# Kernel optimization log

Measured on AMD Instinct MI355X. Metric: run time of the kernel, lower is better.

## Reference

```python
import jax, jax.numpy as jnp
import numpy as np

STATE_DIM = 256
ACTION_DIM = 2
HIDDEN = 512
N_HEADS = 5          # per ensemble; 2*N_HEADS stacked critics total
CEM_POP = 4096
CEM_ITERS = 4
ELITE_N = max(1, int(round(CEM_POP * 0.2)))  # 819
ACTION_LOW, ACTION_HIGH = -1.0, 1.0
INIT_STD, MIN_STD = 0.4, 0.1


def setup_inputs() -> dict:
    key = jax.random.key(0)
    ks = jax.random.split(key, 6)
    in_dim = STATE_DIM + ACTION_DIM
    state = jax.random.normal(ks[0], (1, STATE_DIM), dtype=jnp.float32)
    noise = jax.random.normal(ks[1], (CEM_ITERS, CEM_POP, ACTION_DIM), dtype=jnp.float32)
    W1 = jax.random.normal(ks[2], (2 * N_HEADS, in_dim, HIDDEN), dtype=jnp.float32) / np.sqrt(in_dim).astype(np.float32)
    b1 = jnp.zeros((2 * N_HEADS, HIDDEN), dtype=jnp.float32)
    W2 = jax.random.normal(ks[3], (2 * N_HEADS, HIDDEN, HIDDEN), dtype=jnp.float32) / np.sqrt(HIDDEN).astype(np.float32)
    b2 = jnp.zeros((2 * N_HEADS, HIDDEN), dtype=jnp.float32)
    W3 = jax.random.normal(ks[4], (2 * N_HEADS, HIDDEN, 1), dtype=jnp.float32) / np.sqrt(HIDDEN).astype(np.float32)
    b3 = jnp.zeros((2 * N_HEADS, 1), dtype=jnp.float32)
    return {"state": state, "noise": noise, "W1": W1, "b1": b1, "W2": W2, "b2": b2, "W3": W3, "b3": b3}


def _ensemble_scores(s_batch, a, W1, b1, W2, b2, W3, b3):
    # x: [P, state+action]; heads stacked on leading dim h = 2*N_HEADS
    x = jnp.concatenate([s_batch, a], axis=-1)
    h = jax.nn.relu(jnp.einsum('pi,hij->hpj', x, W1) + b1[:, None, :])
    h = jax.nn.relu(jnp.einsum('hpj,hjk->hpk', h, W2) + b2[:, None, :])
    q = (jnp.einsum('hpk,hko->hpo', h, W3) + b3[:, None, :])[..., 0]  # [2H, P]
    q1, q2 = q[:N_HEADS], q[N_HEADS:]
    return jnp.minimum(q1, q2).mean(axis=0)  # [P]


def reference(state, noise, W1, b1, W2, b2, W3, b3):
    s = state[0]  # squeeze(0)
    s_batch = jnp.broadcast_to(s, (CEM_POP, STATE_DIM))

    def step(carry, eps):
        mu, std, best_a, best_score = carry
        a = jnp.clip(mu + std * eps, ACTION_LOW, ACTION_HIGH)  # [P, A]
        scores = _ensemble_scores(s_batch, a, W1, b1, W2, b2, W3, b3)
        vals, idx = jax.lax.top_k(scores, ELITE_N)
        elite = a[idx]  # [ELITE_N, A]
        mu2 = elite.mean(axis=0)
        std2 = jnp.maximum(jnp.std(elite, axis=0, ddof=1), MIN_STD)  # torch unbiased std
        better = vals[0] > best_score
        best_a2 = jnp.where(better, elite[0], best_a)
        best_score2 = jnp.where(better, vals[0], best_score)
        return (mu2, std2, best_a2, best_score2), None

    carry0 = (jnp.zeros((ACTION_DIM,), jnp.float32),
              jnp.full((ACTION_DIM,), INIT_STD, jnp.float32),
              jnp.zeros((ACTION_DIM,), jnp.float32),
              jnp.float32(-jnp.inf))
    (mu, std, best_a, best_score), _ = jax.lax.scan(step, carry0, noise)
    return best_a[None, :]  # [1, ACTION_DIM]
```

## Files before the change

### kernel.cpp

```cpp
#include <hip/hip_runtime.h>
#include <math.h>

#define SDIM   256
#define HID    512
#define NH     5
#define HEADS  10
#define POP    4096
#define ITERS  4
#define ELITE  819
#define INIT_STDF 0.4f
#define MIN_STDF  0.1f

#define WS_BASE1 0
#define WS_Q     5120
#define WS_STATE 87040
#define WS_W2S_BYTE 348224
#define W2S_USHORTS (HEADS * 2 * 16 * 16384)
#define WS_NEED_BYTES (WS_W2S_BYTE + (size_t)W2S_USHORTS * 2)

typedef __attribute__((ext_vector_type(4))) float f32x4;
typedef __attribute__((ext_vector_type(8))) short bf16x8;

static __device__ __forceinline__ unsigned short bf16_rne(float x) {
    unsigned b = __float_as_uint(x);
    return (unsigned short)((b + 0x7FFFu + ((b >> 16) & 1u)) >> 16);
}

static __device__ __forceinline__ unsigned pack2(float x, float y) {
    unsigned r;
    asm("v_cvt_pk_bf16_f32 %0, %1, %2" : "=v"(r) : "v"(x), "v"(y));
    return r;
}

static __device__ __forceinline__ float clip1(float x) {
    return fminf(fmaxf(x, -1.f), 1.f);
}

__global__ __launch_bounds__(256) void k_base(const float* __restrict__ state,
                                              const float* __restrict__ W1,
                                              const float* __restrict__ b1,
                                              float* __restrict__ ws)
{
    const int h = blockIdx.y;
    const int j = blockIdx.x * 256 + threadIdx.x;
    const float* w1h = W1 + (size_t)h * 258 * HID;
    float acc = b1[h * HID + j];
    for (int i = 0; i < SDIM; ++i)
        acc += state[i] * w1h[(size_t)i * HID + j];
    ws[WS_BASE1 + h * HID + j] = acc;

    if (h == 0 && blockIdx.x == 0 && threadIdx.x == 0) {
        float* st = ws + WS_STATE;
        st[0] = 0.f; st[1] = 0.f;
        st[2] = INIT_STDF; st[3] = INIT_STDF;
        st[4] = 0.f; st[5] = 0.f;
        st[6] = -3.402823466e38f;
    }
}

__global__ __launch_bounds__(256) void k_split(const float* __restrict__ W2,
                                               unsigned short* __restrict__ W2S)
{
    const int h = blockIdx.z, cb = blockIdx.y, jc = blockIdx.x;
    const int c = threadIdx.x;
    unsigned short* slab = W2S + (size_t)((h * 2 + cb) * 16 + jc) * 16384;
    #pragma unroll
    for (int jg = 0; jg < 4; ++jg) {
        unsigned hp[4], lp[4];
        #pragma unroll
        for (int i = 0; i < 4; ++i) {
            const int j = jc * 32 + jg * 8 + 2 * i;
            float v0 = W2[(size_t)(h * HID + j) * HID + cb * 256 + c];
            float v1 = W2[(size_t)(h * HID + j + 1) * HID + cb * 256 + c];
            unsigned short h0 = bf16_rne(v0), h1 = bf16_rne(v1);
            float f0 = __uint_as_float((unsigned)h0 << 16);
            float f1 = __uint_as_float((unsigned)h1 << 16);
            unsigned short l0 = bf16_rne(v0 - f0), l1 = bf16_rne(v1 - f1);
            hp[i] = (unsigned)h0 | ((unsigned)h1 << 16);
            lp[i] = (unsigned)l0 | ((unsigned)l1 << 16);
        }
        uint4 HV, LV;
        HV.x = hp[0]; HV.y = hp[1]; HV.z = hp[2]; HV.w = hp[3];
        LV.x = lp[0]; LV.y = lp[1]; LV.z = lp[2]; LV.w = lp[3];
        *(uint4*)&slab[jg * 2048 + c * 8] = HV;
        *(uint4*)&slab[8192 + jg * 2048 + c * 8] = LV;
    }
}

__global__ __launch_bounds__(512, 4) void k_score_mfma7(
    const float* __restrict__ noise, const float* __restrict__ W1,
    const unsigned short* __restrict__ W2S,
    const float* __restrict__ b2, const float* __restrict__ W3,
    float* __restrict__ ws, int t)
{
    __shared__ unsigned short As[2][4096];
    __shared__ float red[8][64];

    const int tid = threadIdx.x;
    const int bid = blockIdx.x;
    const int w = (bid & 7) * 160 + (bid >> 3);
    const int h = w >> 7;
    const int rem = w & 127;
    const int cb = rem >> 6;
    const int rs = rem & 63;

    const int lane = tid & 63;
    const int wv = tid >> 6;
    const int l15 = lane & 15, lk = lane >> 4;

    const int arow = tid & 63;
    const int akg = (tid >> 6) & 3;

    const float* st = ws + WS_STATE;
    const float mu0 = st[0], mu1 = st[1], sd0 = st[2], sd1 = st[3];
    float2 e = *(const float2*)&noise[((size_t)t * POP + rs * 64 + arow) * 2];
    const float a0 = clip1(mu0 + sd0 * e.x);
    const float a1 = clip1(mu1 + sd1 * e.y);

    const float* base1 = ws + WS_BASE1 + h * HID;
    const float* w1u = W1 + ((size_t)h * 258 + 256) * HID;
    const float* w1v = W1 + ((size_t)h * 258 + 257) * HID;
    const unsigned short* bslab = W2S + (size_t)((h * 2 + cb) * 16) * 16384;
    const int bco = lk * 2048 + (wv * 32 + l15) * 8;

    auto computeA = [&](int jc, int buf) {
        if (tid < 256) {
            const int j = jc * 32 + akg * 8;
            f32x4 b0 = *(const f32x4*)&base1[j];
            f32x4 b1v = *(const f32x4*)&base1[j + 4];
            f32x4 u0 = *(const f32x4*)&w1u[j];
            f32x4 u1 = *(const f32x4*)&w1u[j + 4];
            f32x4 v0 = *(const f32x4*)&w1v[j];
            f32x4 v1 = *(const f32x4*)&w1v[j + 4];
            float hv[8];
            #pragma unroll
            for (int i = 0; i < 4; ++i) {
                hv[i]     = fmaxf(b0[i] + a0 * u0[i] + a1 * v0[i], 0.f);
                hv[4 + i] = fmaxf(b1v[i] + a0 * u1[i] + a1 * v1[i], 0.f);
            }
            unsigned ph[4], pl[4];
            #pragma unroll
            for (int i = 0; i < 4; ++i) {
                ph[i] = pack2(hv[2 * i], hv[2 * i + 1]);
                float fx = __uint_as_float(ph[i] << 16);
                float fy = __uint_as_float(ph[i] & 0xFFFF0000u);
                pl[i] = pack2(hv[2 * i] - fx, hv[2 * i + 1] - fy);
            }
            uint4 HV, LV;
            HV.x = ph[0]; HV.y = ph[1]; HV.z = ph[2]; HV.w = ph[3];
            LV.x = pl[0]; LV.y = pl[1]; LV.z = pl[2]; LV.w = pl[3];
            *(uint4*)&As[buf][akg * 512 + arow * 8] = HV;
            *(uint4*)&As[buf][2048 + akg * 512 + arow * 8] = LV;
        }
    };

    f32x4 acc[4][2];
    #pragma unroll
    for (int m = 0; m < 4; ++m)
        #pragma unroll
        for (int n = 0; n < 2; ++n)
            acc[m][n] = (f32x4){0.f, 0.f, 0.f, 0.f};

    computeA(0, 0);
    bf16x8 BH[2], BL[2];
    #pragma unroll
    for (int n = 0; n < 2; ++n) {
        BH[n] = *(const bf16x8*)(bslab + bco + n * 128);
        BL[n] = *(const bf16x8*)(bslab + 8192 + bco + n * 128);
    }
    __syncthreads();

    int cur = 0;
    #pragma unroll 1
    for (int kc = 0; kc < 16; ++kc) {
        bf16x8 AH[4], AL[4];
        #pragma unroll
        for (int m = 0; m < 4; ++m) {
            const int ad = lk * 512 + (m * 16 + l15) * 8;
            AH[m] = *(const bf16x8*)&As[cur][ad];
            AL[m] = *(const bf16x8*)&As[cur][2048 + ad];
        }
        const int nc = (kc < 15) ? kc + 1 : 15;
        const unsigned short* bnc = bslab + (size_t)nc * 16384;
        bf16x8 nBH[2], nBL[2];
        #pragma unroll
        for (int n = 0; n < 2; ++n) {
            nBH[n] = *(const bf16x8*)(bnc + bco + n * 128);
            nBL[n] = *(const bf16x8*)(bnc + 8192 + bco + n * 128);
        }
        __builtin_amdgcn_s_setprio(1);
        #pragma unroll
        for (int m = 0; m < 4; ++m)
            #pragma unroll
            for (int n = 0; n < 2; ++n)
                acc[m][n] = __builtin_amdgcn_mfma_f32_16x16x32_bf16(
                    AH[m], BH[n], acc[m][n], 0, 0, 0);
        #pragma unroll
        for (int m = 0; m < 4; ++m)
            #pragma unroll
            for (int n = 0; n < 2; ++n)
                acc[m][n] = __builtin_amdgcn_mfma_f32_16x16x32_bf16(
                    AL[m], BH[n], acc[m][n], 0, 0, 0);
        #pragma unroll
        for (int m = 0; m < 4; ++m)
            #pragma unroll
            for (int n = 0; n < 2; ++n)
                acc[m][n] = __builtin_amdgcn_mfma_f32_16x16x32_bf16(
                    AH[m], BL[n], acc[m][n], 0, 0, 0);
        __builtin_amdgcn_s_setprio(0);
        computeA(nc, cur ^ 1);
        __syncthreads();
        #pragma unroll
        for (int n = 0; n < 2; ++n) { BH[n] = nBH[n]; BL[n] = nBL[n]; }
        cur ^= 1;
    }

    float qp[4][4];
    #pragma unroll
    for (int m = 0; m < 4; ++m)
        #pragma unroll
        for (int r = 0; r < 4; ++r) qp[m][r] = 0.f;
    #pragma unroll
    for (int n = 0; n < 2; ++n) {
        int gcol = cb * 256 + wv * 32 + n * 16 + l15;
        float b2v = b2[h * HID + gcol];
        float w3v = W3[h * HID + gcol];
        #pragma unroll
        for (int m = 0; m < 4; ++m)
            #pragma unroll
            for (int r = 0; r < 4; ++r)
                qp[m][r] += fmaxf(acc[m][n][r] + b2v, 0.f) * w3v;
    }
    #pragma unroll
    for (int m = 0; m < 4; ++m)
        #pragma unroll
        for (int r = 0; r < 4; ++r) {
            float v = qp[m][r];
            v += __shfl_xor(v, 1);
            v += __shfl_xor(v, 2);
            v += __shfl_xor(v, 4);
            v += __shfl_xor(v, 8);
            if (l15 == 0) red[wv][m * 16 + lk * 4 + r] = v;
        }
    __syncthreads();
    if (tid < 64) {
        float q = 0.f;
        #pragma unroll
        for (int s = 0; s < 8; ++s) q += red[s][tid];
        ws[WS_Q + (size_t)(cb * HEADS + h) * POP + rs * 64 + tid] = q;
    }
}

__global__ __launch_bounds__(256) void k_score(const float* __restrict__ noise,
                                               const float* __restrict__ W1,
                                               const float* __restrict__ W2,
                                               const float* __restrict__ b2,
                                               const float* __restrict__ W3,
                                               float* __restrict__ ws, int t)
{
    __shared__ float h1[32][HID];
    __shared__ float a0s[32], a1s[32];
    __shared__ float red[2][16][2];

    const int tid = threadIdx.x;
    const int h   = blockIdx.y;
    const int p0  = blockIdx.x * 32;

    if (tid < 32) {
        const float* st = ws + WS_STATE;
        const int p = p0 + tid;
        float e0 = noise[((size_t)t * POP + p) * 2 + 0];
        float e1 = noise[((size_t)t * POP + p) * 2 + 1];
        a0s[tid] = fminf(fmaxf(st[0] + st[2] * e0, -1.f), 1.f);
        a1s[tid] = fminf(fmaxf(st[1] + st[3] * e1, -1.f), 1.f);
    }
    __syncthreads();

    const float* base1 = ws + WS_BASE1 + h * HID;
    const float* w1u = W1 + ((size_t)h * 258 + 256) * HID;
    const float* w1v = W1 + ((size_t)h * 258 + 257) * HID;
    #pragma unroll
    for (int jj = 0; jj < 2; ++jj) {
        int j = tid + jj * 256;
        float bb = base1[j], uu = w1u[j], vv = w1v[j];
        #pragma unroll
        for (int p = 0; p < 32; ++p)
            h1[p][j] = fmaxf(bb + a0s[p] * uu + a1s[p] * vv, 0.f);
    }
    __syncthreads();

    const int pg = tid >> 7;
    const int kl = tid & 127;
    const float* W2h = W2 + (size_t)h * HID * HID + kl;

    float acc[16][4];
    #pragma unroll
    for (int p = 0; p < 16; ++p)
        #pragma unroll
        for (int dk = 0; dk < 4; ++dk) acc[p][dk] = 0.f;

    for (int j0 = 0; j0 < HID; j0 += 4) {
        float w[4][4];
        #pragma unroll
        for (int dj = 0; dj < 4; ++dj)
            #pragma unroll
            for (int dk = 0; dk < 4; ++dk)
                w[dj][dk] = W2h[(size_t)(j0 + dj) * HID + dk * 128];
        #pragma unroll
        for (int p = 0; p < 16; ++p) {
            const float4 hv = *(const float4*)&h1[pg * 16 + p][j0];
            #pragma unroll
            for (int dk = 0; dk < 4; ++dk)
                acc[p][dk] += hv.x * w[0][dk] + hv.y * w[1][dk]
                            + hv.z * w[2][dk] + hv.w * w[3][dk];
        }
    }

    float b2v[4], w3v[4];
    #pragma unroll
    for (int dk = 0; dk < 4; ++dk) {
        b2v[dk] = b2[h * HID + kl + dk * 128];
        w3v[dk] = W3[h * HID + kl + dk * 128];
    }
    const int wid  = tid >> 6;
    const int lane = tid & 63;
    const int wig  = wid & 1;
    #pragma unroll
    for (int p = 0; p < 16; ++p) {
        float v = 0.f;
        #pragma unroll
        for (int dk = 0; dk < 4; ++dk)
            v += fmaxf(acc[p][dk] + b2v[dk], 0.f) * w3v[dk];
        #pragma unroll
        for (int off = 32; off; off >>= 1) v += __shfl_down(v, off);
        if (lane == 0) red[pg][p][wig] = v;
    }
    __syncthreads();
    if (tid < 32) {
        int pp = tid & 15, g = tid >> 4;
        ws[WS_Q + (size_t)h * POP + p0 + g * 16 + pp] =
            red[g][pp][0] + red[g][pp][1];
        ws[WS_Q + (size_t)(HEADS + h) * POP + p0 + g * 16 + pp] = 0.f;
    }
}

__global__ __launch_bounds__(256) void k_select(const float* __restrict__ noise,
                                                const float* __restrict__ b3,
                                                float* __restrict__ ws,
                                                float* __restrict__ out, int t)
{
    __shared__ float    sc[POP];
    __shared__ unsigned uk[POP];
    __shared__ unsigned hist[256];
    __shared__ int      scan[256];
    __shared__ float    rf[256];
    __shared__ int      ri_[256];
    __shared__ double   rd[256];
    __shared__ unsigned s_prefix;
    __shared__ int      s_r;

    const int tid = threadIdx.x;
    const float* q = ws + WS_Q;
    float* st = ws + WS_STATE;
    const float mu0 = st[0], mu1 = st[1], sd0 = st[2], sd1 = st[3];

    #pragma unroll
    for (int g = 0; g < 4; ++g) {
        const int p = g * 1024 + tid * 4;
        f32x4 s = (f32x4){0.f, 0.f, 0.f, 0.f};
        #pragma unroll
        for (int hh = 0; hh < NH; ++hh) {
            f32x4 qa0 = *(const f32x4*)&q[(size_t)hh * POP + p];
            f32x4 qa1 = *(const f32x4*)&q[(size_t)(HEADS + hh) * POP + p];
            f32x4 qb0 = *(const f32x4*)&q[(size_t)(NH + hh) * POP + p];
            f32x4 qb1 = *(const f32x4*)&q[(size_t)(HEADS + NH + hh) * POP + p];
            float ba = b3[hh], bb = b3[NH + hh];
            #pragma unroll
            for (int i = 0; i < 4; ++i)
                s[i] += fminf(qa0[i] + qa1[i] + ba, qb0[i] + qb1[i] + bb);
        }
        #pragma unroll
        for (int i = 0; i < 4; ++i) {
            float v = s[i] * 0.2f;
            sc[p + i] = v;
            unsigned b = __float_as_uint(v);
            uk[p + i] = (b & 0x80000000u) ? ~b : (b | 0x80000000u);
        }
    }
    __syncthreads();

    float mv = -3.402823466e38f; int mi = 0;
    for (int p = tid; p < POP; p += 256) {
        float v = sc[p];
        if (v > mv) { mv = v; mi = p; }
    }
    rf[tid] = mv; ri_[tid] = mi;
    __syncthreads();
    for (int off = 128; off; off >>= 1) {
        if (tid < off) {
            float ov = rf[tid + off]; int oi = ri_[tid + off];
            if (ov > rf[tid] || (ov == rf[tid] && oi < ri_[tid])) {
                rf[tid] = ov; ri_[tid] = oi;
            }
        }
        __syncthreads();
    }
    const float maxsc = rf[0];
    const int argmax = ri_[0];
    __syncthreads();

    unsigned prefix = 0; int r = ELITE;
    for (int shift = 24; shift >= 0; shift -= 8) {
        hist[tid] = 0;
        __syncthreads();
        const unsigned himask = (shift < 24) ? (0xFFFFFFFFu << (shift + 8)) : 0u;
        for (int p = tid; p < POP; p += 256) {
            unsigned key = uk[p];
            if ((key & himask) == prefix)
                atomicAdd(&hist[(key >> shift) & 255u], 1u);
        }
        __syncthreads();
        scan[tid] = (int)hist[tid];
        __syncthreads();
        for (int off = 1; off < 256; off <<= 1) {
            int v = (tid + off < 256) ? scan[tid + off] : 0;
            __syncthreads();
            scan[tid] += v;
            __syncthreads();
        }
        int above = (tid < 255) ? scan[tid + 1] : 0;
        if (scan[tid] >= r && above < r) {
            s_prefix = prefix | ((unsigned)tid << shift);
            s_r = r - above;
        }
        __syncthreads();
        prefix = s_prefix; r = s_r;
        __syncthreads();
    }
    const unsigned uT = prefix;
    const int take = r;

    int tieloc = 0;
    {
        const int base = tid * 16;
        #pragma unroll
        for (int k = 0; k < 16; ++k) if (uk[base + k] == uT) tieloc++;
    }
    scan[tid] = tieloc;
    __syncthreads();
    for (int off = 1; off < 256; off <<= 1) {
        int v = (tid >= off) ? scan[tid - off] : 0;
        __syncthreads();
        scan[tid] += v;
        __syncthreads();
    }
    const int tieExcl = scan[tid] - tieloc;

    double s0 = 0, s1 = 0, ss0 = 0, ss1 = 0;
    {
        const int base = tid * 16;
        int trank = tieExcl;
        for (int k = 0; k < 16; ++k) {
            const int p = base + k;
            const unsigned key = uk[p];
            bool inc = false;
            if (key > uT) inc = true;
            else if (key == uT) { if (trank < take) inc = true; trank++; }
            if (inc) {
                float e0 = noise[((size_t)t * POP + p) * 2 + 0];
                float e1 = noise[((size_t)t * POP + p) * 2 + 1];
                float a0 = fminf(fmaxf(mu0 + sd0 * e0, -1.f), 1.f);
                float a1 = fminf(fmaxf(mu1 + sd1 * e1, -1.f), 1.f);
                s0 += a0; s1 += a1;
                ss0 += (double)a0 * a0; ss1 += (double)a1 * a1;
            }
        }
    }
    double S0, S1, SS0, SS1;
    rd[tid] = s0;  __syncthreads();
    for (int off = 128; off; off >>= 1) { if (tid < off) rd[tid] += rd[tid + off]; __syncthreads(); }
    S0 = rd[0]; __syncthreads();
    rd[tid] = s1;  __syncthreads();
    for (int off = 128; off; off >>= 1) { if (tid < off) rd[tid] += rd[tid + off]; __syncthreads(); }
    S1 = rd[0]; __syncthreads();
    rd[tid] = ss0; __syncthreads();
    for (int off = 128; off; off >>= 1) { if (tid < off) rd[tid] += rd[tid + off]; __syncthreads(); }
    SS0 = rd[0]; __syncthreads();
    rd[tid] = ss1; __syncthreads();
    for (int off = 128; off; off >>= 1) { if (tid < off) rd[tid] += rd[tid + off]; __syncthreads(); }
    SS1 = rd[0]; __syncthreads();

    if (tid == 0) {
        const double n = (double)ELITE;
        double m0 = S0 / n, m1 = S1 / n;
        double v0 = (SS0 - S0 * S0 / n) / (n - 1.0);
        double v1 = (SS1 - S1 * S1 / n) / (n - 1.0);
        float nsd0 = fmaxf((float)sqrt(fmax(v0, 0.0)), MIN_STDF);
        float nsd1 = fmaxf((float)sqrt(fmax(v1, 0.0)), MIN_STDF);
        float e0 = noise[((size_t)t * POP + argmax) * 2 + 0];
        float e1 = noise[((size_t)t * POP + argmax) * 2 + 1];
        float a0 = fminf(fmaxf(mu0 + sd0 * e0, -1.f), 1.f);
        float a1 = fminf(fmaxf(mu1 + sd1 * e1, -1.f), 1.f);
        if (maxsc > st[6]) { st[4] = a0; st[5] = a1; st[6] = maxsc; }
        st[0] = (float)m0; st[1] = (float)m1; st[2] = nsd0; st[3] = nsd1;
        if (t == ITERS - 1) { out[0] = st[4]; out[1] = st[5]; }
    }
}

extern "C" void kernel_launch(void* const* d_in, const int* in_sizes, int n_in,
                              void* d_out, int out_size, void* d_ws, size_t ws_size,
                              hipStream_t stream)
{
    const float* state = (const float*)d_in[0];
    const float* noise = (const float*)d_in[1];
    const float* W1    = (const float*)d_in[2];
    const float* b1    = (const float*)d_in[3];
    const float* W2    = (const float*)d_in[4];
    const float* b2    = (const float*)d_in[5];
    const float* W3    = (const float*)d_in[6];
    const float* b3    = (const float*)d_in[7];
    float* out = (float*)d_out;
    float* ws  = (float*)d_ws;

    const bool fast = ws_size >= WS_NEED_BYTES;

    k_base<<<dim3(2, HEADS), 256, 0, stream>>>(state, W1, b1, ws);
    if (fast) {
        unsigned short* W2S = (unsigned short*)((char*)d_ws + WS_W2S_BYTE);
        k_split<<<dim3(16, 2, HEADS), 256, 0, stream>>>(W2, W2S);
        for (int t = 0; t < ITERS; ++t) {
            k_score_mfma7<<<dim3(1280), 512, 0, stream>>>(
                noise, W1, W2S, b2, W3, ws, t);
            k_select<<<1, 256, 0, stream>>>(noise, b3, ws, out, t);
        }
    } else {
        for (int t = 0; t < ITERS; ++t) {
            k_score<<<dim3(POP / 32, HEADS), 256, 0, stream>>>(noise, W1, W2, b2, W3, ws, t);
            k_select<<<1, 256, 0, stream>>>(noise, b3, ws, out, t);
        }
    }
}
```

Before: 344.3 us.

## Switch scoring GEMM to 32x32x16 MFMA and widen select kernel to 1024 threads

The scoring kernel's inner product moves from 16x16x32 bf16 MFMA tiles to 32x32x16 tiles. It uses 16-wide accumulators and new A/B fragment addressing, which cuts the number of MFMA issues and LDS fragment loads per K-chunk. The epilogue reduction adds one more shuffle stage and remaps rows to fit the 32x32 output layout. Separately, the single-block top-k/select kernel grows from 256 to 1024 threads so each thread does less serial work, at the cost of longer scans and reductions and heavier barriers.

```diff
diff --git a/kernel.cpp b/kernel.cpp
--- a/kernel.cpp
+++ b/kernel.cpp
@@ -19,6 +19,7 @@
 #define WS_NEED_BYTES (WS_W2S_BYTE + (size_t)W2S_USHORTS * 2)
 
 typedef __attribute__((ext_vector_type(4))) float f32x4;
+typedef __attribute__((ext_vector_type(16))) float f32x16;
 typedef __attribute__((ext_vector_type(8))) short bf16x8;
 
 static __device__ __forceinline__ unsigned short bf16_rne(float x) {
@@ -87,7 +88,7 @@
     }
 }
 
-__global__ __launch_bounds__(512, 4) void k_score_mfma7(
+__global__ __launch_bounds__(512, 4) void k_score_mfma8(
     const float* __restrict__ noise, const float* __restrict__ W1,
     const unsigned short* __restrict__ W2S,
     const float* __restrict__ b2, const float* __restrict__ W3,
@@ -106,7 +107,8 @@
 
     const int lane = tid & 63;
     const int wv = tid >> 6;
-    const int l15 = lane & 15, lk = lane >> 4;
+    const int l31 = lane & 31;
+    const int lg = lane >> 5;
 
     const int arow = tid & 63;
     const int akg = (tid >> 6) & 3;
@@ -121,7 +123,8 @@
     const float* w1u = W1 + ((size_t)h * 258 + 256) * HID;
     const float* w1v = W1 + ((size_t)h * 258 + 257) * HID;
     const unsigned short* bslab = W2S + (size_t)((h * 2 + cb) * 16) * 16384;
-    const int bco = lk * 2048 + (wv * 32 + l15) * 8;
+    const int bco = lg * 2048 + (wv * 32 + l31) * 8;
+    const int ar0 = lg * 512 + l31 * 8;
 
     auto computeA = [&](int jc, int buf) {
         if (tid < 256) {
@@ -154,93 +157,83 @@
         }
     };
 
-    f32x4 acc[4][2];
-    #pragma unroll
-    for (int m = 0; m < 4; ++m)
-        #pragma unroll
-        for (int n = 0; n < 2; ++n)
-            acc[m][n] = (f32x4){0.f, 0.f, 0.f, 0.f};
+    f32x16 acc[2];
+    #pragma unroll
+    for (int mi = 0; mi < 2; ++mi)
+        #pragma unroll
+        for (int i = 0; i < 16; ++i) acc[mi][i] = 0.f;
 
     computeA(0, 0);
     bf16x8 BH[2], BL[2];
     #pragma unroll
-    for (int n = 0; n < 2; ++n) {
-        BH[n] = *(const bf16x8*)(bslab + bco + n * 128);
-        BL[n] = *(const bf16x8*)(bslab + 8192 + bco + n * 128);
+    for (int ks = 0; ks < 2; ++ks) {
+        BH[ks] = *(const bf16x8*)(bslab + bco + ks * 4096);
+        BL[ks] = *(const bf16x8*)(bslab + 8192 + bco + ks * 4096);
     }
     __syncthreads();
 
     int cur = 0;
     #pragma unroll 1
     for (int kc = 0; kc < 16; ++kc) {
-        bf16x8 AH[4], AL[4];
-        #pragma unroll
-        for (int m = 0; m < 4; ++m) {
-            const int ad = lk * 512 + (m * 16 + l15) * 8;
-            AH[m] = *(const bf16x8*)&As[cur][ad];
-            AL[m] = *(const bf16x8*)&As[cur][2048 + ad];
-        }
+        bf16x8 AH[2][2], AL[2][2];
+        #pragma unroll
+        for (int ks = 0; ks < 2; ++ks)
+            #pragma unroll
+            for (int mi = 0; mi < 2; ++mi) {
+                const int ad = ar0 + ks * 1024 + mi * 256;
+                AH[ks][mi] = *(const bf16x8*)&As[cur][ad];
+                AL[ks][mi] = *(const bf16x8*)&As[cur][2048 + ad];
+            }
         const int nc = (kc < 15) ? kc + 1 : 15;
         const unsigned short* bnc = bslab + (size_t)nc * 16384;
         bf16x8 nBH[2], nBL[2];
         #pragma unroll
-        for (int n = 0; n < 2; ++n) {
-            nBH[n] = *(const bf16x8*)(bnc + bco + n * 128);
-            nBL[n] = *(const bf16x8*)(bnc + 8192 + bco + n * 128);
+        for (int ks = 0; ks < 2; ++ks) {
+            nBH[ks] = *(const bf16x8*)(bnc + bco + ks * 4096);
+            nBL[ks] = *(const bf16x8*)(bnc + 8192 + bco + ks * 4096);
         }
         __builtin_amdgcn_s_setprio(1);
         #pragma unroll
-        for (int m = 0; m < 4; ++m)
-            #pragma unroll
-            for (int n = 0; n < 2; ++n)
-                acc[m][n] = __builtin_amdgcn_mfma_f32_16x16x32_bf16(
-                    AH[m], BH[n], acc[m][n], 0, 0, 0);
-        #pragma unroll
-        for (int m = 0; m < 4; ++m)
-            #pragma unroll
-            for (int n = 0; n < 2; ++n)
-                acc[m][n] = __builtin_amdgcn_mfma_f32_16x16x32_bf16(
-                    AL[m], BH[n], acc[m][n], 0, 0, 0);
-        #pragma unroll
-        for (int m = 0; m < 4; ++m)
-            #pragma unroll
-            for (int n = 0; n < 2; ++n)
-                acc[m][n] = __builtin_amdgcn_mfma_f32_16x16x32_bf16(
-                    AH[m], BL[n], acc[m][n], 0, 0, 0);
+        for (int ks = 0; ks < 2; ++ks)
+            #pragma unroll
+            for (int mi = 0; mi < 2; ++mi)
+                acc[mi] = __builtin_amdgcn_mfma_f32_32x32x16_bf16(
+                    AH[ks][mi], BH[ks], acc[mi], 0, 0, 0);
+        #pragma unroll
+        for (int ks = 0; ks < 2; ++ks)
+            #pragma unroll
+            for (int mi = 0; mi < 2; ++mi)
+                acc[mi] = __builtin_amdgcn_mfma_f32_32x32x16_bf16(
+                    AL[ks][mi], BH[ks], acc[mi], 0, 0, 0);
+        #pragma unroll
+        for (int ks = 0; ks < 2; ++ks)
+            #pragma unroll
+            for (int mi = 0; mi < 2; ++mi)
+                acc[mi] = __builtin_amdgcn_mfma_f32_32x32x16_bf16(
+                    AH[ks][mi], BL[ks], acc[mi], 0, 0, 0);
         __builtin_amdgcn_s_setprio(0);
         computeA(nc, cur ^ 1);
         __syncthreads();
         #pragma unroll
-        for (int n = 0; n < 2; ++n) { BH[n] = nBH[n]; BL[n] = nBL[n]; }
+        for (int ks = 0; ks < 2; ++ks) { BH[ks] = nBH[ks]; BL[ks] = nBL[ks]; }
         cur ^= 1;
     }
 
-    float qp[4][4];
-    #pragma unroll
-    for (int m = 0; m < 4; ++m)
-        #pragma unroll
-        for (int r = 0; r < 4; ++r) qp[m][r] = 0.f;
-    #pragma unroll
-    for (int n = 0; n < 2; ++n) {
-        int gcol = cb * 256 + wv * 32 + n * 16 + l15;
-        float b2v = b2[h * HID + gcol];
-        float w3v = W3[h * HID + gcol];
-        #pragma unroll
-        for (int m = 0; m < 4; ++m)
-            #pragma unroll
-            for (int r = 0; r < 4; ++r)
-                qp[m][r] += fmaxf(acc[m][n][r] + b2v, 0.f) * w3v;
-    }
-    #pragma unroll
-    for (int m = 0; m < 4; ++m)
-        #pragma unroll
-        for (int r = 0; r < 4; ++r) {
-            float v = qp[m][r];
+    const int gcol = cb * 256 + wv * 32 + l31;
+    const float b2v = b2[h * HID + gcol];
+    const float w3v = W3[h * HID + gcol];
+    #pragma unroll
+    for (int mi = 0; mi < 2; ++mi)
+        #pragma unroll
+        for (int r = 0; r < 16; ++r) {
+            float v = fmaxf(acc[mi][r] + b2v, 0.f) * w3v;
             v += __shfl_xor(v, 1);
             v += __shfl_xor(v, 2);
             v += __shfl_xor(v, 4);
             v += __shfl_xor(v, 8);
-            if (l15 == 0) red[wv][m * 16 + lk * 4 + r] = v;
+            v += __shfl_xor(v, 16);
+            if (l31 == 0)
+                red[wv][mi * 32 + (r & 3) + 8 * (r >> 2) + 4 * lg] = v;
         }
     __syncthreads();
     if (tid < 64) {
@@ -344,18 +337,18 @@
     }
 }
 
-__global__ __launch_bounds__(256) void k_select(const float* __restrict__ noise,
-                                                const float* __restrict__ b3,
-                                                float* __restrict__ ws,
-                                                float* __restrict__ out, int t)
+__global__ __launch_bounds__(1024) void k_select(const float* __restrict__ noise,
+                                                 const float* __restrict__ b3,
+                                                 float* __restrict__ ws,
+                                                 float* __restrict__ out, int t)
 {
     __shared__ float    sc[POP];
     __shared__ unsigned uk[POP];
     __shared__ unsigned hist[256];
-    __shared__ int      scan[256];
-    __shared__ float    rf[256];
-    __shared__ int      ri_[256];
-    __shared__ double   rd[256];
+    __shared__ int      scan2[1024];
+    __shared__ float    rf[1024];
+    __shared__ int      ri_[1024];
+    __shared__ double   rd[1024];
     __shared__ unsigned s_prefix;
     __shared__ int      s_r;
 
@@ -364,9 +357,8 @@
     float* st = ws + WS_STATE;
     const float mu0 = st[0], mu1 = st[1], sd0 = st[2], sd1 = st[3];
 
-    #pragma unroll
-    for (int g = 0; g < 4; ++g) {
-        const int p = g * 1024 + tid * 4;
+    {
+        const int p = tid * 4;
         f32x4 s = (f32x4){0.f, 0.f, 0.f, 0.f};
         #pragma unroll
         for (int hh = 0; hh < NH; ++hh) {
@@ -390,13 +382,15 @@
     __syncthreads();
 
     float mv = -3.402823466e38f; int mi = 0;
-    for (int p = tid; p < POP; p += 256) {
+    #pragma unroll
+    for (int k = 0; k < 4; ++k) {
+        const int p = tid * 4 + k;
         float v = sc[p];
         if (v > mv) { mv = v; mi = p; }
     }
     rf[tid] = mv; ri_[tid] = mi;
     __syncthreads();
-    for (int off = 128; off; off >>= 1) {
+    for (int off = 512; off; off >>= 1) {
         if (tid < off) {
             float ov = rf[tid + off]; int oi = ri_[tid + off];
             if (ov > rf[tid] || (ov == rf[tid] && oi < ri_[tid])) {
@@ -411,27 +405,29 @@
 
     unsigned prefix = 0; int r = ELITE;
     for (int shift = 24; shift >= 0; shift -= 8) {
-        hist[tid] = 0;
+        if (tid < 256) hist[tid] = 0;
         __syncthreads();
         const unsigned himask = (shift < 24) ? (0xFFFFFFFFu << (shift + 8)) : 0u;
-        for (int p = tid; p < POP; p += 256) {
+        for (int p = tid; p < POP; p += 1024) {
             unsigned key = uk[p];
             if ((key & himask) == prefix)
                 atomicAdd(&hist[(key >> shift) & 255u], 1u);
         }
         __syncthreads();
-        scan[tid] = (int)hist[tid];
+        scan2[tid] = (tid < 256) ? (int)hist[tid] : 0;
         __syncthreads();
         for (int off = 1; off < 256; off <<= 1) {
-            int v = (tid + off < 256) ? scan[tid + off] : 0;
+            int v = (tid < 256 && tid + off < 256) ? scan2[tid + off] : 0;
             __syncthreads();
-            scan[tid] += v;
+            if (tid < 256) scan2[tid] += v;
             __syncthreads();
         }
-        int above = (tid < 255) ? scan[tid + 1] : 0;
-        if (scan[tid] >= r && above < r) {
-            s_prefix = prefix | ((unsigned)tid << shift);
-            s_r = r - above;
+        if (tid < 256) {
+            int above = (tid < 255) ? scan2[tid + 1] : 0;
+            if (scan2[tid] >= r && above < r) {
+                s_prefix = prefix | ((unsigned)tid << shift);
+                s_r = r - above;
+            }
         }
         __syncthreads();
         prefix = s_prefix; r = s_r;
@@ -442,25 +438,26 @@
 
     int tieloc = 0;
     {
-        const int base = tid * 16;
-        #pragma unroll
-        for (int k = 0; k < 16; ++k) if (uk[base + k] == uT) tieloc++;
-    }
-    scan[tid] = tieloc;
-    __syncthreads();
-    for (int off = 1; off < 256; off <<= 1) {
-        int v = (tid >= off) ? scan[tid - off] : 0;
-        __syncthreads();
-        scan[tid] += v;
-        __syncthreads();
-    }
-    const int tieExcl = scan[tid] - tieloc;
+        const int base = tid * 4;
+        #pragma unroll
+        for (int k = 0; k < 4; ++k) if (uk[base + k] == uT) tieloc++;
+    }
+    scan2[tid] = tieloc;
+    __syncthreads();
+    for (int off = 1; off < 1024; off <<= 1) {
+        int v = (tid >= off) ? scan2[tid - off] : 0;
+        __syncthreads();
+        scan2[tid] += v;
+        __syncthreads();
+    }
+    const int tieExcl = scan2[tid] - tieloc;
 
     double s0 = 0, s1 = 0, ss0 = 0, ss1 = 0;
     {
-        const int base = tid * 16;
+        const int base = tid * 4;
         int trank = tieExcl;
-        for (int k = 0; k < 16; ++k) {
+        #pragma unroll
+        for (int k = 0; k < 4; ++k) {
             const int p = base + k;
             const unsigned key = uk[p];
             bool inc = false;
@@ -478,16 +475,16 @@
     }
     double S0, S1, SS0, SS1;
     rd[tid] = s0;  __syncthreads();
-    for (int off = 128; off; off >>= 1) { if (tid < off) rd[tid] += rd[tid + off]; __syncthreads(); }
+    for (int off = 512; off; off >>= 1) { if (tid < off) rd[tid] += rd[tid + off]; __syncthreads(); }
     S0 = rd[0]; __syncthreads();
     rd[tid] = s1;  __syncthreads();
-    for (int off = 128; off; off >>= 1) { if (tid < off) rd[tid] += rd[tid + off]; __syncthreads(); }
+    for (int off = 512; off; off >>= 1) { if (tid < off) rd[tid] += rd[tid + off]; __syncthreads(); }
     S1 = rd[0]; __syncthreads();
     rd[tid] = ss0; __syncthreads();
-    for (int off = 128; off; off >>= 1) { if (tid < off) rd[tid] += rd[tid + off]; __syncthreads(); }
+    for (int off = 512; off; off >>= 1) { if (tid < off) rd[tid] += rd[tid + off]; __syncthreads(); }
     SS0 = rd[0]; __syncthreads();
     rd[tid] = ss1; __syncthreads();
-    for (int off = 128; off; off >>= 1) { if (tid < off) rd[tid] += rd[tid + off]; __syncthreads(); }
+    for (int off = 512; off; off >>= 1) { if (tid < off) rd[tid] += rd[tid + off]; __syncthreads(); }
     SS1 = rd[0]; __syncthreads();
 
     if (tid == 0) {
@@ -529,14 +526,14 @@
         unsigned short* W2S = (unsigned short*)((char*)d_ws + WS_W2S_BYTE);
         k_split<<<dim3(16, 2, HEADS), 256, 0, stream>>>(W2, W2S);
         for (int t = 0; t < ITERS; ++t) {
-            k_score_mfma7<<<dim3(1280), 512, 0, stream>>>(
+            k_score_mfma8<<<dim3(1280), 512, 0, stream>>>(
                 noise, W1, W2S, b2, W3, ws, t);
-            k_select<<<1, 256, 0, stream>>>(noise, b3, ws, out, t);
+            k_select<<<1, 1024, 0, stream>>>(noise, b3, ws, out, t);
         }
     } else {
         for (int t = 0; t < ITERS; ++t) {
             k_score<<<dim3(POP / 32, HEADS), 256, 0, stream>>>(noise, W1, W2, b2, W3, ws, t);
-            k_select<<<1, 256, 0, stream>>>(noise, b3, ws, out, t);
-        }
-    }
-}
+            k_select<<<1, 1024, 0, stream>>>(noise, b3, ws, out, t);
+        }
+    }
+}
```

New measurement: 416.5 us. +21.0%, slower.
